# Kernel optimization log

Measured on AMD Instinct MI355X. Metric: run time of the kernel, lower is better.

The kernel has to match this reference:

```python
import jax, jax.numpy as jnp
import numpy as np

B, LQ, LK = 8, 1024, 1024
H, HD = 8, 128            # n_head, hidden_dim (per-head)
HEAD_DIM, CHILD_DIM = 512, 512
D_MODEL = HEAD_DIM + CHILD_DIM
TEMP = float(np.sqrt(HD))
NEG = 100000000.0
EPS = 1e-5


def setup_inputs() -> dict:
    key = jax.random.key(0)
    ks = jax.random.split(key, 12)
    q = jax.random.normal(ks[0], (B, LQ, HEAD_DIM), jnp.float32)
    k = jax.random.normal(ks[1], (B, LK, CHILD_DIM), jnp.float32)
    v = jax.random.normal(ks[2], (B, LK, D_MODEL), jnp.float32)
    old_score = 0.1 * jax.random.normal(ks[3], (H * B, LQ, LK), jnp.float32)
    float_mask = (jax.random.uniform(ks[4], (B, LQ, LK)) > 0.2).astype(jnp.float32)
    # torch nn.Linear weights are [out_features, in_features]
    wq = jax.random.normal(ks[5], (H * HD, HEAD_DIM), jnp.float32) * np.sqrt(2.0 / (HEAD_DIM + HD))
    wk = jax.random.normal(ks[6], (H * HD, CHILD_DIM), jnp.float32) * np.sqrt(2.0 / (CHILD_DIM + HD))
    wv = jax.random.normal(ks[7], (H * HD, D_MODEL), jnp.float32) * np.sqrt(2.0 / (D_MODEL + HD))
    wfc = jax.random.normal(ks[8], (D_MODEL, H * HD), jnp.float32) * np.sqrt(2.0 / (D_MODEL + H * HD))
    bq = jnp.zeros((H * HD,), jnp.float32)
    bk = jnp.zeros((H * HD,), jnp.float32)
    bv = jnp.zeros((H * HD,), jnp.float32)
    bfc = jnp.zeros((D_MODEL,), jnp.float32)
    ln_g = jnp.ones((D_MODEL,), jnp.float32)
    ln_b = jnp.zeros((D_MODEL,), jnp.float32)
    return dict(q=q, k=k, v=v, old_score=old_score, float_mask=float_mask,
                wq=wq, bq=bq, wk=wk, bk=bk, wv=wv, bv=bv,
                wfc=wfc, bfc=bfc, ln_g=ln_g, ln_b=ln_b)


def reference(q, k, v, old_score, float_mask, wq, bq, wk, bk, wv, bv, wfc, bfc, ln_g, ln_b):
    b, lq, _ = q.shape
    lk = k.shape[1]
    residual = v
    qh = (q @ wq.T + bq).reshape(b, lq, H, HD)   # [b,lq,h,d]
    kh = (k @ wk.T + bk).reshape(b, lk, H, HD)
    vh = (v @ wv.T + bv).reshape(b, lk, H, HD)
    # raw_score laid out head-major to match torch's (n_head*B, Lq, Lk)
    raw = jnp.einsum('bqhd,bkhd->hbqk', qh, kh) + old_score.reshape(H, b, lq, lk)
    score = raw - NEG * (1.0 - float_mask)[None]          # broadcast over heads
    attn = jax.nn.softmax(score / TEMP, axis=-1)          # eval path
    out = jnp.einsum('hbqk,bkhd->bqhd', attn, vh).reshape(b, lq, H * HD)
    out = out @ wfc.T + bfc + residual                    # dropout=identity (eval)
    mean = jnp.mean(out, axis=-1, keepdims=True)
    var = jnp.mean(jnp.square(out - mean), axis=-1, keepdims=True)
    out = (out - mean) / jnp.sqrt(var + EPS) * ln_g + ln_b
    return out, raw.reshape(H * b, lq, lk)
```

## Files before the change

### kernel.cpp

```cpp
#include <hip/hip_runtime.h>

typedef unsigned short u16;
typedef __bf16 bf16x8 __attribute__((ext_vector_type(8)));
typedef float f32x4 __attribute__((ext_vector_type(4)));

#define MFMA16(a,b,c) __builtin_amdgcn_mfma_f32_16x16x32_bf16(a,b,c,0,0,0)
#define WAITV(n) asm volatile("s_waitcnt vmcnt(" #n ")" ::: "memory")
#define SBAR()   __builtin_amdgcn_s_barrier()
#define SCHED0() __builtin_amdgcn_sched_barrier(0)

static __device__ __forceinline__ u16 f2bf(float f){
  unsigned u = __builtin_bit_cast(unsigned, f);
  u += 0x7fffu + ((u>>16)&1u);
  return (u16)(u>>16);
}
static __device__ __forceinline__ int swz256(int r,int c){ return r*256 + (c ^ ((r&7)<<4)); }
static __device__ __forceinline__ int swz128(int r,int c){ return r*128 + (c ^ ((r&7)<<4)); }

static __device__ __forceinline__ void gload16(const void* g, void* l){
  __builtin_amdgcn_global_load_lds(
      (const __attribute__((address_space(1))) unsigned int*)g,
      (__attribute__((address_space(3))) unsigned int*)l, 16, 0, 0);
}

__global__ void conv_f2b(const float* __restrict__ in, u16* __restrict__ out, int n4){
  int i = blockIdx.x*256 + threadIdx.x;
  if (i >= n4) return;
  float4 f = reinterpret_cast<const float4*>(in)[i];
  ushort4 o; o.x=f2bf(f.x); o.y=f2bf(f.y); o.z=f2bf(f.z); o.w=f2bf(f.w);
  reinterpret_cast<ushort4*>(out)[i] = o;
}

__global__ void mask2bits(const float* __restrict__ fm, unsigned char* __restrict__ bits){
  int i = blockIdx.x*256 + threadIdx.x;
  const float4* p = reinterpret_cast<const float4*>(fm + (size_t)i*8);
  float4 a = p[0], bq = p[1];
  unsigned v = 0;
  v |= (a.x  > 0.5f) ? 1u   : 0u;
  v |= (a.y  > 0.5f) ? 2u   : 0u;
  v |= (a.z  > 0.5f) ? 4u   : 0u;
  v |= (a.w  > 0.5f) ? 8u   : 0u;
  v |= (bq.x > 0.5f) ? 16u  : 0u;
  v |= (bq.y > 0.5f) ? 32u  : 0u;
  v |= (bq.z > 0.5f) ? 64u  : 0u;
  v |= (bq.w > 0.5f) ? 128u : 0u;
  bits[i] = (unsigned char)v;
}

template<int MODE>
__global__ __launch_bounds__(256) void gemm_nt(const u16* __restrict__ A, const u16* __restrict__ Bw,
    const float* __restrict__ bias, const float* __restrict__ resid,
    u16* __restrict__ Cb, float* __restrict__ Cf, int M, int N, int K)
{
  __shared__ uint4 ldsv[2048];
  char* la = (char*)ldsv;
  char* lb = la + 16384;
  const int tid = threadIdx.x, lane = tid&63, w = tid>>6;
  const int l15 = lane&15, l4 = lane>>4;
  const int wm = w&1, wn = w>>1;
  const int mb = blockIdx.x, nb = blockIdx.y;
  const f32x4 zero4 = {0.f,0.f,0.f,0.f};
  f32x4 acc[4][4];
  #pragma unroll
  for (int i=0;i<4;++i)
    #pragma unroll
    for (int j=0;j<4;++j) acc[i][j] = zero4;

  for (int k0=0;k0<K;k0+=64){
    __syncthreads();
    #pragma unroll
    for (int it=0; it<4; ++it){
      int slot = it*256 + tid;
      int r = slot>>3, cg = (slot&7) ^ (r&7);
      gload16(A + (size_t)(mb*128+r)*K + k0 + cg*8, la + (it*256 + w*64)*16);
      gload16(Bw + (size_t)(nb*128+r)*K + k0 + cg*8, lb + (it*256 + w*64)*16);
    }
    __syncthreads();
    #pragma unroll
    for (int kk=0;kk<2;++kk){
      bf16x8 af[4], bfr[4];
      #pragma unroll
      for (int i=0;i<4;++i){
        af[i]  = *reinterpret_cast<const bf16x8*>(la + swz128(wm*64+i*16+l15, (kk*32+l4*8)*2));
        bfr[i] = *reinterpret_cast<const bf16x8*>(lb + swz128(wn*64+i*16+l15, (kk*32+l4*8)*2));
      }
      #pragma unroll
      for (int i=0;i<4;++i)
        #pragma unroll
        for (int j=0;j<4;++j)
          acc[i][j] = MFMA16(af[i], bfr[j], acc[i][j]);
    }
  }
  #pragma unroll
  for (int j=0;j<4;++j){
    int col = nb*128 + wn*64 + j*16 + l15;
    float bv = bias[col];
    #pragma unroll
    for (int i=0;i<4;++i){
      int row0 = mb*128 + wm*64 + i*16 + l4*4;
      if (MODE == 0){
        #pragma unroll
        for (int r=0;r<4;++r)
          Cb[(size_t)(row0+r)*N + col] = f2bf(acc[i][j][r] + bv);
      } else if (MODE == 1){
        int bb = row0 >> 10, kp = row0 & 1023;
        ushort4 o;
        o.x = f2bf(acc[i][j][0]+bv); o.y = f2bf(acc[i][j][1]+bv);
        o.z = f2bf(acc[i][j][2]+bv); o.w = f2bf(acc[i][j][3]+bv);
        *reinterpret_cast<ushort4*>(Cb + (size_t)(bb*1024+col)*1024 + kp) = o;
      } else {
        #pragma unroll
        for (int r=0;r<4;++r){
          size_t off = (size_t)(row0+r)*N + col;
          Cf[off] = acc[i][j][r] + bv + resid[off];
        }
      }
    }
  }
}

__global__ __launch_bounds__(256) void attn_fused(const u16* __restrict__ qh,
    const u16* __restrict__ kh, const u16* __restrict__ vt,
    const float* __restrict__ oldsc, const unsigned char* __restrict__ bits,
    float* __restrict__ raw, u16* __restrict__ ao)
{
  __shared__ uint4 ldsv[4608];
  char* lk0 = (char*)ldsv;
  char* lv0 = lk0 + 16384;
  char* lk1 = lk0 + 32768;
  char* lv1 = lk0 + 49152;
  char* lp_ = lk0 + 65536;
  const int tid = threadIdx.x, lane = tid&63, w = tid>>6;
  const int l15 = lane&15, l4 = lane>>4;
  unsigned ublk = blockIdx.x;
  int slotid = (ublk & 7) * 128 + (ublk >> 3);
  const int qb = slotid & 15, bh = slotid >> 4;
  const int b = bh & 7, h = bh >> 3;
  const float invT = 0.088388347648318447f;
  const f32x4 zero4 = {0.f,0.f,0.f,0.f};

  const int qglob = qb*64 + w*16 + l4*4;
  const float* oldp = oldsc + ((size_t)(h*8+b)*1024 + qglob)*1024 + l15*4;
  float*       rawp = raw   + ((size_t)(h*8+b)*1024 + qglob)*1024 + l15*4;
  const unsigned char* bitp = bits + ((size_t)b*1024 + qglob)*128 + (l15>>1);
  const u16* khB = kh + (size_t)b*1024*1024 + h*128;
  const u16* vtB = vt + ((size_t)b*1024 + h*128)*1024;
  const int nsh = (l15&1)*4;

  bf16x8 qf[4];
  {
    const u16* qp = qh + (size_t)(b*1024 + qb*64 + w*16 + l15)*1024 + h*128 + l4*8;
    #pragma unroll
    for (int kk=0;kk<4;++kk)
      qf[kk] = __builtin_bit_cast(bf16x8, *reinterpret_cast<const uint4*>(qp + kk*32));
  }
  f32x4 oacc[8];
  #pragma unroll
  for (int i=0;i<8;++i) oacc[i] = zero4;
  float mr[4], lr[4];
  #pragma unroll
  for (int r=0;r<4;++r){ mr[r] = -3.0e38f; lr[r] = 0.f; }

  auto stage = [&](int kt, char* lkD, char* lvD){
    #pragma unroll
    for (int it=0; it<4; ++it){
      int slot = it*256 + tid;
      int rs = slot>>4, cs = slot&15;
      int ck = cs ^ (rs&7);
      int kv = (rs&15)*4 + (rs>>4);
      gload16(khB + (size_t)(kt*64 + kv)*1024 + ck*8, lkD + (it*256 + w*64)*16);
      int r8 = slot>>3, cgv = (slot&7) ^ (r8&7);
      gload16(vtB + (size_t)r8*1024 + kt*64 + cgv*8, lvD + (it*256 + w*64)*16);
    }
  };
  auto pref = [&](int kt, float4 (&o4)[4], unsigned char (&bb)[4]){
    #pragma unroll
    for (int r=0;r<4;++r){
      o4[r] = *reinterpret_cast<const float4*>(oldp + (size_t)r*1024 + kt*64);
      bb[r] = bitp[(size_t)r*128 + kt*8];
    }
  };
  auto body = [&](int kt, char* lkR, char* lvR, float4 (&o4)[4], unsigned char (&bb)[4]){
    f32x4 fs[4];
    #pragma unroll
    for (int fj=0;fj<4;++fj){
      f32x4 s = zero4;
      #pragma unroll
      for (int kk=0;kk<4;++kk){
        bf16x8 kf = *reinterpret_cast<const bf16x8*>(lkR + swz256(fj*16+l15, (kk*32+l4*8)*2));
        s = MFMA16(qf[kk], kf, s);
      }
      fs[fj] = s;
    }
    float tm[4];
    #pragma unroll
    for (int r=0;r<4;++r){
      float4 rv;
      rv.x = fs[0][r] + o4[r].x; rv.y = fs[1][r] + o4[r].y;
      rv.z = fs[2][r] + o4[r].z; rv.w = fs[3][r] + o4[r].w;
      *reinterpret_cast<float4*>(rawp + (size_t)r*1024 + kt*64) = rv;
      unsigned nib = ((unsigned)bb[r]) >> nsh;
      fs[0][r] = (rv.x - ((nib&1u) ? 0.f : 1.0e8f)) * invT;
      fs[1][r] = (rv.y - ((nib&2u) ? 0.f : 1.0e8f)) * invT;
      fs[2][r] = (rv.z - ((nib&4u) ? 0.f : 1.0e8f)) * invT;
      fs[3][r] = (rv.w - ((nib&8u) ? 0.f : 1.0e8f)) * invT;
      tm[r] = fmaxf(fmaxf(fs[0][r], fs[1][r]), fmaxf(fs[2][r], fs[3][r]));
    }
    #pragma unroll
    for (int o=1;o<16;o<<=1){
      #pragma unroll
      for (int r=0;r<4;++r) tm[r] = fmaxf(tm[r], __shfl_xor(tm[r], o));
    }
    #pragma unroll
    for (int r=0;r<4;++r){
      float mn  = fmaxf(mr[r], tm[r]);
      float esc = __expf(mr[r] - mn);
      mr[r] = mn;
      lr[r] *= esc;
      #pragma unroll
      for (int nf=0;nf<8;++nf) oacc[nf][r] *= esc;
      float px = __expf(fs[0][r] - mn), py = __expf(fs[1][r] - mn);
      float pz = __expf(fs[2][r] - mn), pw = __expf(fs[3][r] - mn);
      lr[r] += px + py + pz + pw;
      ushort4 o;
      o.x = f2bf(px); o.y = f2bf(py); o.z = f2bf(pz); o.w = f2bf(pw);
      int prow = w*16 + l4*4 + r;
      *reinterpret_cast<ushort4*>(lp_ + swz128(prow, l15*8)) = o;
    }
    #pragma unroll
    for (int kkv=0;kkv<2;++kkv){
      bf16x8 pf = *reinterpret_cast<const bf16x8*>(lp_ + swz128(w*16+l15, (kkv*32+l4*8)*2));
      #pragma unroll
      for (int nf=0;nf<8;++nf){
        bf16x8 vf = *reinterpret_cast<const bf16x8*>(lvR + swz128(nf*16+l15, (kkv*32+l4*8)*2));
        oacc[nf] = MFMA16(pf, vf, oacc[nf]);
      }
    }
  };

  float4 oA[4], oB[4];
  unsigned char bA[4], bB[4];
  stage(0, lk0, lv0);
  stage(1, lk1, lv1);
  pref(0, oA, bA);
  pref(1, oB, bB);
  WAITV(8);
  SBAR(); SCHED0();
  body(0, lk0, lv0, oA, bA);
  pref(2, oA, bA);

  #pragma unroll 1
  for (int t = 1; t <= 13; t += 2){
    SBAR();
    stage(t+1, lk0, lv0);
    WAITV(16);
    SBAR(); SCHED0();
    body(t, lk1, lv1, oB, bB);
    if (t+2 <= 15) pref(t+2, oB, bB);
    SBAR();
    stage(t+2, lk1, lv1);
    WAITV(16);
    SBAR(); SCHED0();
    body(t+1, lk0, lv0, oA, bA);
    if (t+3 <= 15) pref(t+3, oA, bA);
  }
  SBAR();
  WAITV(0);
  SBAR(); SCHED0();
  body(15, lk1, lv1, oB, bB);

  #pragma unroll
  for (int o=1;o<16;o<<=1){
    #pragma unroll
    for (int r=0;r<4;++r) lr[r] += __shfl_xor(lr[r], o);
  }
  #pragma unroll
  for (int nf=0;nf<8;++nf){
    int col = h*128 + nf*16 + l15;
    #pragma unroll
    for (int r=0;r<4;++r){
      size_t orow = (size_t)(b*1024 + qb*64 + w*16 + l4*4 + r);
      ao[orow*1024 + col] = f2bf(oacc[nf][r] * (1.0f/lr[r]));
    }
  }
}

__global__ __launch_bounds__(256) void ln_k(float* __restrict__ io,
    const float* __restrict__ g, const float* __restrict__ bb)
{
  const int lane = threadIdx.x & 63, w = threadIdx.x >> 6;
  size_t row = (size_t)blockIdx.x*4 + w;
  float4* p = reinterpret_cast<float4*>(io + row*1024);
  float4 x[4];
  float s = 0.f, s2 = 0.f;
  #pragma unroll
  for (int i=0;i<4;++i){
    x[i] = p[lane + i*64];
    s  += x[i].x + x[i].y + x[i].z + x[i].w;
    s2 += x[i].x*x[i].x + x[i].y*x[i].y + x[i].z*x[i].z + x[i].w*x[i].w;
  }
  #pragma unroll
  for (int o=1;o<64;o<<=1){ s += __shfl_xor(s,o); s2 += __shfl_xor(s2,o); }
  float mean = s * 0.0009765625f;
  float var  = s2 * 0.0009765625f - mean*mean;
  float rstd = rsqrtf(var + 1e-5f);
  const float4* gp = reinterpret_cast<const float4*>(g);
  const float4* bp = reinterpret_cast<const float4*>(bb);
  #pragma unroll
  for (int i=0;i<4;++i){
    float4 gg = gp[lane+i*64], bv = bp[lane+i*64], y;
    y.x = (x[i].x-mean)*rstd*gg.x + bv.x;
    y.y = (x[i].y-mean)*rstd*gg.y + bv.y;
    y.z = (x[i].z-mean)*rstd*gg.z + bv.z;
    y.w = (x[i].w-mean)*rstd*gg.w + bv.w;
    p[lane+i*64] = y;
  }
}

extern "C" void kernel_launch(void* const* d_in, const int* in_sizes, int n_in,
                              void* d_out, int out_size, void* d_ws, size_t ws_size,
                              hipStream_t stream)
{
  const float* q    = (const float*)d_in[0];
  const float* k    = (const float*)d_in[1];
  const float* v    = (const float*)d_in[2];
  const float* olds = (const float*)d_in[3];
  const float* fm   = (const float*)d_in[4];
  const float* wq   = (const float*)d_in[5];
  const float* bq   = (const float*)d_in[6];
  const float* wk   = (const float*)d_in[7];
  const float* bk   = (const float*)d_in[8];
  const float* wv   = (const float*)d_in[9];
  const float* bv   = (const float*)d_in[10];
  const float* wfc  = (const float*)d_in[11];
  const float* bfc  = (const float*)d_in[12];
  const float* lng  = (const float*)d_in[13];
  const float* lnb  = (const float*)d_in[14];
  float* out = (float*)d_out;
  float* raw = out + 8388608;

  u16* ws  = (u16*)d_ws;
  u16* qbf = ws;
  u16* kbf = qbf + 4194304;
  u16* vbf = kbf + 4194304;
  u16* wqb = vbf + 8388608;
  u16* wkb = wqb + 524288;
  u16* wvb = wkb + 524288;
  u16* wfb = wvb + 1048576;
  u16* qhb = wfb + 1048576;
  u16* khb = qhb + 8388608;
  u16* vtb = khb + 8388608;
  u16* aob = vtb + 8388608;
  unsigned char* bits = (unsigned char*)(aob + 8388608);

  conv_f2b<<<4096,256,0,stream>>>(q,   qbf, 1048576);
  conv_f2b<<<4096,256,0,stream>>>(k,   kbf, 1048576);
  conv_f2b<<<8192,256,0,stream>>>(v,   vbf, 2097152);
  conv_f2b<<<512, 256,0,stream>>>(wq,  wqb, 131072);
  conv_f2b<<<512, 256,0,stream>>>(wk,  wkb, 131072);
  conv_f2b<<<1024,256,0,stream>>>(wv,  wvb, 262144);
  conv_f2b<<<1024,256,0,stream>>>(wfc, wfb, 262144);
  mask2bits<<<4096,256,0,stream>>>(fm, bits);

  gemm_nt<0><<<dim3(64,8),256,0,stream>>>(qbf, wqb, bq, nullptr, qhb, nullptr, 8192,1024,512);
  gemm_nt<0><<<dim3(64,8),256,0,stream>>>(kbf, wkb, bk, nullptr, khb, nullptr, 8192,1024,512);
  gemm_nt<1><<<dim3(64,8),256,0,stream>>>(vbf, wvb, bv, nullptr, vtb, nullptr, 8192,1024,1024);

  attn_fused<<<1024,256,0,stream>>>(qhb, khb, vtb, olds, bits, raw, aob);

  gemm_nt<2><<<dim3(64,8),256,0,stream>>>(aob, wfb, bfc, v, nullptr, out, 8192,1024,1024);
  ln_k<<<2048,256,0,stream>>>(out, lng, lnb);
}
```

Baseline: 303.4 us.

## Repack mask bits per column group, deepen prefetch, skip uneeded softmax rescales

The mask bit layout changes so each lane fetches one 32-bit word holding four rows' bits instead of four separate byte loads. The fused attention loop now prefetches old_score and mask three tiles ahead with a third register set, unrolled by six, to hide global load latency. The online softmax skips the running-max update and accumulator rescale when no row's new max exceeds the old by more than 8, which trades a small exponent headroom for fewer multiplies. The changes add register pressure and more intricate vmcnt wait counts that must match the number of loads in flight.

Measured after the change: 331.2 us. 1.09x slower.

```diff
diff --git a/kernel.cpp b/kernel.cpp
--- a/kernel.cpp
+++ b/kernel.cpp
@@ -31,20 +31,30 @@
   reinterpret_cast<ushort4*>(out)[i] = o;
 }
 
-__global__ void mask2bits(const float* __restrict__ fm, unsigned char* __restrict__ bits){
-  int i = blockIdx.x*256 + threadIdx.x;
-  const float4* p = reinterpret_cast<const float4*>(fm + (size_t)i*8);
-  float4 a = p[0], bq = p[1];
-  unsigned v = 0;
-  v |= (a.x  > 0.5f) ? 1u   : 0u;
-  v |= (a.y  > 0.5f) ? 2u   : 0u;
-  v |= (a.z  > 0.5f) ? 4u   : 0u;
-  v |= (a.w  > 0.5f) ? 8u   : 0u;
-  v |= (bq.x > 0.5f) ? 16u  : 0u;
-  v |= (bq.y > 0.5f) ? 32u  : 0u;
-  v |= (bq.z > 0.5f) ? 64u  : 0u;
-  v |= (bq.w > 0.5f) ? 128u : 0u;
-  bits[i] = (unsigned char)v;
+__global__ void mask2bits(const float* __restrict__ fm, unsigned* __restrict__ bitsW){
+  int T = blockIdx.x*256 + threadIdx.x;
+  int c = T & 127;
+  int q4g = (T >> 7) & 255;
+  int b = T >> 15;
+  int q0 = q4g*4;
+  const float* src = fm + ((size_t)(b*1024 + q0))*1024 + c*8;
+  unsigned out = 0;
+  #pragma unroll
+  for (int r=0;r<4;++r){
+    const float4* p = reinterpret_cast<const float4*>(src + (size_t)r*1024);
+    float4 a = p[0], bq = p[1];
+    unsigned v = 0;
+    v |= (a.x  > 0.5f) ? 1u   : 0u;
+    v |= (a.y  > 0.5f) ? 2u   : 0u;
+    v |= (a.z  > 0.5f) ? 4u   : 0u;
+    v |= (a.w  > 0.5f) ? 8u   : 0u;
+    v |= (bq.x > 0.5f) ? 16u  : 0u;
+    v |= (bq.y > 0.5f) ? 32u  : 0u;
+    v |= (bq.z > 0.5f) ? 64u  : 0u;
+    v |= (bq.w > 0.5f) ? 128u : 0u;
+    out |= v << (r*8);
+  }
+  bitsW[(size_t)(b*128 + c)*256 + q4g] = out;
 }
 
 template<int MODE>
@@ -142,7 +152,7 @@
   const int qglob = qb*64 + w*16 + l4*4;
   const float* oldp = oldsc + ((size_t)(h*8+b)*1024 + qglob)*1024 + l15*4;
   float*       rawp = raw   + ((size_t)(h*8+b)*1024 + qglob)*1024 + l15*4;
-  const unsigned char* bitp = bits + ((size_t)b*1024 + qglob)*128 + (l15>>1);
+  const unsigned char* bitbase = bits + (size_t)b*131072 + (l15>>1)*1024 + qglob;
   const u16* khB = kh + (size_t)b*1024*1024 + h*128;
   const u16* vtB = vt + ((size_t)b*1024 + h*128)*1024;
   const int nsh = (l15&1)*4;
@@ -159,7 +169,7 @@
   for (int i=0;i<8;++i) oacc[i] = zero4;
   float mr[4], lr[4];
   #pragma unroll
-  for (int r=0;r<4;++r){ mr[r] = -3.0e38f; lr[r] = 0.f; }
+  for (int r=0;r<4;++r){ mr[r] = -1.0e30f; lr[r] = 0.f; }
 
   auto stage = [&](int kt, char* lkD, char* lvD){
     #pragma unroll
@@ -173,14 +183,13 @@
       gload16(vtB + (size_t)r8*1024 + kt*64 + cgv*8, lvD + (it*256 + w*64)*16);
     }
   };
-  auto pref = [&](int kt, float4 (&o4)[4], unsigned char (&bb)[4]){
-    #pragma unroll
-    for (int r=0;r<4;++r){
+  auto pref = [&](int kt, float4 (&o4)[4], unsigned &bw){
+    #pragma unroll
+    for (int r=0;r<4;++r)
       o4[r] = *reinterpret_cast<const float4*>(oldp + (size_t)r*1024 + kt*64);
-      bb[r] = bitp[(size_t)r*128 + kt*8];
-    }
+    bw = *reinterpret_cast<const unsigned*>(bitbase + (size_t)kt*8192);
   };
-  auto body = [&](int kt, char* lkR, char* lvR, float4 (&o4)[4], unsigned char (&bb)[4]){
+  auto body = [&](int kt, char* lkR, char* lvR, float4 (&o4)[4], unsigned bw){
     f32x4 fs[4];
     #pragma unroll
     for (int fj=0;fj<4;++fj){
@@ -199,7 +208,7 @@
       rv.x = fs[0][r] + o4[r].x; rv.y = fs[1][r] + o4[r].y;
       rv.z = fs[2][r] + o4[r].z; rv.w = fs[3][r] + o4[r].w;
       *reinterpret_cast<float4*>(rawp + (size_t)r*1024 + kt*64) = rv;
-      unsigned nib = ((unsigned)bb[r]) >> nsh;
+      unsigned nib = bw >> (r*8 + nsh);
       fs[0][r] = (rv.x - ((nib&1u) ? 0.f : 1.0e8f)) * invT;
       fs[1][r] = (rv.y - ((nib&2u) ? 0.f : 1.0e8f)) * invT;
       fs[2][r] = (rv.z - ((nib&4u) ? 0.f : 1.0e8f)) * invT;
@@ -211,16 +220,22 @@
       #pragma unroll
       for (int r=0;r<4;++r) tm[r] = fmaxf(tm[r], __shfl_xor(tm[r], o));
     }
+    float dmax = fmaxf(fmaxf(tm[0]-mr[0], tm[1]-mr[1]), fmaxf(tm[2]-mr[2], tm[3]-mr[3]));
+    if (!__all((int)(dmax <= 8.0f))){
+      #pragma unroll
+      for (int r=0;r<4;++r){
+        float mn  = fmaxf(mr[r], tm[r]);
+        float esc = __expf(mr[r] - mn);
+        lr[r] *= esc;
+        #pragma unroll
+        for (int nf=0;nf<8;++nf) oacc[nf][r] *= esc;
+        mr[r] = mn;
+      }
+    }
     #pragma unroll
     for (int r=0;r<4;++r){
-      float mn  = fmaxf(mr[r], tm[r]);
-      float esc = __expf(mr[r] - mn);
-      mr[r] = mn;
-      lr[r] *= esc;
-      #pragma unroll
-      for (int nf=0;nf<8;++nf) oacc[nf][r] *= esc;
-      float px = __expf(fs[0][r] - mn), py = __expf(fs[1][r] - mn);
-      float pz = __expf(fs[2][r] - mn), pw = __expf(fs[3][r] - mn);
+      float px = __expf(fs[0][r] - mr[r]), py = __expf(fs[1][r] - mr[r]);
+      float pz = __expf(fs[2][r] - mr[r]), pw = __expf(fs[3][r] - mr[r]);
       lr[r] += px + py + pz + pw;
       ushort4 o;
       o.x = f2bf(px); o.y = f2bf(py); o.z = f2bf(pz); o.w = f2bf(pw);
@@ -238,36 +253,47 @@
     }
   };
 
-  float4 oA[4], oB[4];
-  unsigned char bA[4], bB[4];
+  float4 oA[4], oB[4], oC[4];
+  unsigned bwA, bwB, bwC;
+
   stage(0, lk0, lv0);
   stage(1, lk1, lv1);
-  pref(0, oA, bA);
-  pref(1, oB, bB);
-  WAITV(8);
+  pref(0, oA, bwA);
+  pref(1, oB, bwB);
+  pref(2, oC, bwC);
+  WAITV(10);
   SBAR(); SCHED0();
-  body(0, lk0, lv0, oA, bA);
-  pref(2, oA, bA);
+  body(0, lk0, lv0, oA, bwA);
+  pref(3, oA, bwA);
+
+  SBAR();
+  stage(2, lk0, lv0);
+  WAITV(17); SBAR(); SCHED0();
+  body(1, lk1, lv1, oB, bwB);
+  pref(4, oB, bwB);
+
+#define ATT_STEP(T, LKr, LVr, LKs, LVs, OS, BWS, DOPREF) \
+  SBAR(); stage((T)+1, LKs, LVs); WAITV(17); SBAR(); SCHED0(); \
+  body((T), LKr, LVr, OS, BWS); if (DOPREF) pref((T)+3, OS, BWS);
 
   #pragma unroll 1
-  for (int t = 1; t <= 13; t += 2){
-    SBAR();
-    stage(t+1, lk0, lv0);
-    WAITV(16);
-    SBAR(); SCHED0();
-    body(t, lk1, lv1, oB, bB);
-    if (t+2 <= 15) pref(t+2, oB, bB);
-    SBAR();
-    stage(t+2, lk1, lv1);
-    WAITV(16);
-    SBAR(); SCHED0();
-    body(t+1, lk0, lv0, oA, bA);
-    if (t+3 <= 15) pref(t+3, oA, bA);
-  }
+  for (int tb = 2; tb <= 8; tb += 6){
+    ATT_STEP(tb+0, lk0,lv0, lk1,lv1, oC,bwC, true)
+    ATT_STEP(tb+1, lk1,lv1, lk0,lv0, oA,bwA, true)
+    ATT_STEP(tb+2, lk0,lv0, lk1,lv1, oB,bwB, true)
+    ATT_STEP(tb+3, lk1,lv1, lk0,lv0, oC,bwC, true)
+    ATT_STEP(tb+4, lk0,lv0, lk1,lv1, oA,bwA, true)
+    ATT_STEP(tb+5, lk1,lv1, lk0,lv0, oB,bwB, (tb+8 <= 15))
+  }
+#undef ATT_STEP
+
   SBAR();
-  WAITV(0);
-  SBAR(); SCHED0();
-  body(15, lk1, lv1, oB, bB);
+  stage(15, lk1, lv1);
+  WAITV(12); SBAR(); SCHED0();
+  body(14, lk0, lv0, oC, bwC);
+  SBAR();
+  WAITV(4); SBAR(); SCHED0();
+  body(15, lk1, lv1, oA, bwA);
 
   #pragma unroll
   for (int o=1;o<16;o<<=1){
@@ -360,7 +386,7 @@
   conv_f2b<<<512, 256,0,stream>>>(wk,  wkb, 131072);
   conv_f2b<<<1024,256,0,stream>>>(wv,  wvb, 262144);
   conv_f2b<<<1024,256,0,stream>>>(wfc, wfb, 262144);
-  mask2bits<<<4096,256,0,stream>>>(fm, bits);
+  mask2bits<<<1024,256,0,stream>>>(fm, (unsigned*)bits);
 
   gemm_nt<0><<<dim3(64,8),256,0,stream>>>(qbf, wqb, bq, nullptr, qhb, nullptr, 8192,1024,512);
   gemm_nt<0><<<dim3(64,8),256,0,stream>>>(kbf, wkb, bk, nullptr, khb, nullptr, 8192,1024,512);
```

## Software-pipeline attention: overlap QK of next tile with PV of previous

Applied to the files above, without the earlier changes.

Restructures the attention loop so the K and V tiles are staged separately and the P·V product of tile t-1 runs alongside the QK product of tile t, with double-buffered P in LDS. It also adds a lazy-rescale rule that skips the online-softmax rescale of the accumulators when the wavefront's max grows by at most 8, and merges four weight-conversion launches into a single kernel. The aim is to hide the softmax and barrier latency behind matrix-core work and to cut launch overhead. The cost is more LDS per block, which can lower occupancy, and more complex wait-count bookkeeping.

New measurement: 329.3 us. 8.5% more time.

```diff
diff --git a/kernel.cpp b/kernel.cpp
--- a/kernel.cpp
+++ b/kernel.cpp
@@ -29,6 +29,21 @@
   float4 f = reinterpret_cast<const float4*>(in)[i];
   ushort4 o; o.x=f2bf(f.x); o.y=f2bf(f.y); o.z=f2bf(f.z); o.w=f2bf(f.w);
   reinterpret_cast<ushort4*>(out)[i] = o;
+}
+
+__global__ void conv_w(const float* __restrict__ wq, const float* __restrict__ wk,
+                       const float* __restrict__ wv, const float* __restrict__ wfc,
+                       u16* __restrict__ wqb, u16* __restrict__ wkb,
+                       u16* __restrict__ wvb, u16* __restrict__ wfb){
+  int i = blockIdx.x*256 + threadIdx.x;
+  const float* s; u16* d; int off;
+  if (i < 131072)      { s=wq;  d=wqb; off=i; }
+  else if (i < 262144) { s=wk;  d=wkb; off=i-131072; }
+  else if (i < 524288) { s=wv;  d=wvb; off=i-262144; }
+  else                 { s=wfc; d=wfb; off=i-524288; }
+  float4 f = reinterpret_cast<const float4*>(s)[off];
+  ushort4 o; o.x=f2bf(f.x); o.y=f2bf(f.y); o.z=f2bf(f.z); o.w=f2bf(f.w);
+  reinterpret_cast<ushort4*>(d)[off] = o;
 }
 
 __global__ void mask2bits(const float* __restrict__ fm, unsigned char* __restrict__ bits){
@@ -124,12 +139,13 @@
     const float* __restrict__ oldsc, const unsigned char* __restrict__ bits,
     float* __restrict__ raw, u16* __restrict__ ao)
 {
-  __shared__ uint4 ldsv[4608];
+  __shared__ uint4 ldsv[5120];
   char* lk0 = (char*)ldsv;
-  char* lv0 = lk0 + 16384;
-  char* lk1 = lk0 + 32768;
+  char* lk1 = lk0 + 16384;
+  char* lv0 = lk0 + 32768;
   char* lv1 = lk0 + 49152;
-  char* lp_ = lk0 + 65536;
+  char* lp0 = lk0 + 65536;
+  char* lp1 = lk0 + 73728;
   const int tid = threadIdx.x, lane = tid&63, w = tid>>6;
   const int l15 = lane&15, l4 = lane>>4;
   unsigned ublk = blockIdx.x;
@@ -161,7 +177,7 @@
   #pragma unroll
   for (int r=0;r<4;++r){ mr[r] = -3.0e38f; lr[r] = 0.f; }
 
-  auto stage = [&](int kt, char* lkD, char* lvD){
+  auto stageK = [&](int kt, char* lkD){
     #pragma unroll
     for (int it=0; it<4; ++it){
       int slot = it*256 + tid;
@@ -169,6 +185,12 @@
       int ck = cs ^ (rs&7);
       int kv = (rs&15)*4 + (rs>>4);
       gload16(khB + (size_t)(kt*64 + kv)*1024 + ck*8, lkD + (it*256 + w*64)*16);
+    }
+  };
+  auto stageV = [&](int kt, char* lvD){
+    #pragma unroll
+    for (int it=0; it<4; ++it){
+      int slot = it*256 + tid;
       int r8 = slot>>3, cgv = (slot&7) ^ (r8&7);
       gload16(vtB + (size_t)r8*1024 + kt*64 + cgv*8, lvD + (it*256 + w*64)*16);
     }
@@ -180,8 +202,7 @@
       bb[r] = bitp[(size_t)r*128 + kt*8];
     }
   };
-  auto body = [&](int kt, char* lkR, char* lvR, float4 (&o4)[4], unsigned char (&bb)[4]){
-    f32x4 fs[4];
+  auto qk = [&](char* lkR, f32x4 (&fs)[4]){
     #pragma unroll
     for (int fj=0;fj<4;++fj){
       f32x4 s = zero4;
@@ -192,6 +213,19 @@
       }
       fs[fj] = s;
     }
+  };
+  auto pv = [&](char* lvR, char* lpR){
+    #pragma unroll
+    for (int kkv=0;kkv<2;++kkv){
+      bf16x8 pf = *reinterpret_cast<const bf16x8*>(lpR + swz128(w*16+l15, (kkv*32+l4*8)*2));
+      #pragma unroll
+      for (int nf=0;nf<8;++nf){
+        bf16x8 vf = *reinterpret_cast<const bf16x8*>(lvR + swz128(nf*16+l15, (kkv*32+l4*8)*2));
+        oacc[nf] = MFMA16(pf, vf, oacc[nf]);
+      }
+    }
+  };
+  auto sm = [&](int kt, f32x4 (&fs)[4], float4 (&o4)[4], unsigned char (&bb)[4], char* lpW){
     float tm[4];
     #pragma unroll
     for (int r=0;r<4;++r){
@@ -211,63 +245,79 @@
       #pragma unroll
       for (int r=0;r<4;++r) tm[r] = fmaxf(tm[r], __shfl_xor(tm[r], o));
     }
+    float dmax = fmaxf(fmaxf(tm[0]-mr[0], tm[1]-mr[1]), fmaxf(tm[2]-mr[2], tm[3]-mr[3]));
+    if (!__all((int)(dmax <= 8.0f))){
+      #pragma unroll
+      for (int r=0;r<4;++r){
+        float mn  = fmaxf(mr[r], tm[r]);
+        float esc = __expf(mr[r] - mn);
+        lr[r] *= esc;
+        #pragma unroll
+        for (int nf=0;nf<8;++nf) oacc[nf][r] *= esc;
+        mr[r] = mn;
+      }
+    }
     #pragma unroll
     for (int r=0;r<4;++r){
-      float mn  = fmaxf(mr[r], tm[r]);
-      float esc = __expf(mr[r] - mn);
-      mr[r] = mn;
-      lr[r] *= esc;
-      #pragma unroll
-      for (int nf=0;nf<8;++nf) oacc[nf][r] *= esc;
-      float px = __expf(fs[0][r] - mn), py = __expf(fs[1][r] - mn);
-      float pz = __expf(fs[2][r] - mn), pw = __expf(fs[3][r] - mn);
+      float px = __expf(fs[0][r] - mr[r]), py = __expf(fs[1][r] - mr[r]);
+      float pz = __expf(fs[2][r] - mr[r]), pw = __expf(fs[3][r] - mr[r]);
       lr[r] += px + py + pz + pw;
       ushort4 o;
       o.x = f2bf(px); o.y = f2bf(py); o.z = f2bf(pz); o.w = f2bf(pw);
       int prow = w*16 + l4*4 + r;
-      *reinterpret_cast<ushort4*>(lp_ + swz128(prow, l15*8)) = o;
-    }
-    #pragma unroll
-    for (int kkv=0;kkv<2;++kkv){
-      bf16x8 pf = *reinterpret_cast<const bf16x8*>(lp_ + swz128(w*16+l15, (kkv*32+l4*8)*2));
-      #pragma unroll
-      for (int nf=0;nf<8;++nf){
-        bf16x8 vf = *reinterpret_cast<const bf16x8*>(lvR + swz128(nf*16+l15, (kkv*32+l4*8)*2));
-        oacc[nf] = MFMA16(pf, vf, oacc[nf]);
-      }
+      *reinterpret_cast<ushort4*>(lpW + swz128(prow, l15*8)) = o;
     }
   };
 
   float4 oA[4], oB[4];
   unsigned char bA[4], bB[4];
-  stage(0, lk0, lv0);
-  stage(1, lk1, lv1);
+
+  stageK(0, lk0);
   pref(0, oA, bA);
   pref(1, oB, bB);
-  WAITV(8);
+  WAITV(10);
   SBAR(); SCHED0();
-  body(0, lk0, lv0, oA, bA);
-  pref(2, oA, bA);
+
+  {
+    stageK(1, lk1); stageV(0, lv0); SCHED0();
+    f32x4 fs[4];
+    qk(lk0, fs);
+    sm(0, fs, oA, bA, lp0);
+    pref(2, oA, bA);
+    WAITV(9); SBAR(); SCHED0();
+  }
 
   #pragma unroll 1
   for (int t = 1; t <= 13; t += 2){
-    SBAR();
-    stage(t+1, lk0, lv0);
-    WAITV(16);
-    SBAR(); SCHED0();
-    body(t, lk1, lv1, oB, bB);
-    if (t+2 <= 15) pref(t+2, oB, bB);
-    SBAR();
-    stage(t+2, lk1, lv1);
-    WAITV(16);
-    SBAR(); SCHED0();
-    body(t+1, lk0, lv0, oA, bA);
-    if (t+3 <= 15) pref(t+3, oA, bA);
-  }
-  SBAR();
-  WAITV(0);
-  SBAR(); SCHED0();
-  body(15, lk1, lv1, oB, bB);
+    {
+      stageK(t+1, lk0); stageV(t, lv1); SCHED0();
+      f32x4 fs[4];
+      qk(lk1, fs);
+      pv(lv0, lp0);
+      sm(t, fs, oB, bB, lp1);
+      pref(t+2, oB, bB);
+      WAITV(9); SBAR(); SCHED0();
+    }
+    {
+      stageK(t+2, lk1); stageV(t+1, lv0); SCHED0();
+      f32x4 fs[4];
+      qk(lk0, fs);
+      pv(lv1, lp1);
+      sm(t+1, fs, oA, bA, lp0);
+      pref(t+3 <= 15 ? t+3 : 15, oA, bA);
+      WAITV(9); SBAR(); SCHED0();
+    }
+  }
+
+  {
+    stageV(15, lv1); SCHED0();
+    f32x4 fs[4];
+    qk(lk1, fs);
+    pv(lv0, lp0);
+    sm(15, fs, oB, bB, lp1);
+    WAITV(4); SBAR(); SCHED0();
+    pv(lv1, lp1);
+  }
 
   #pragma unroll
   for (int o=1;o<16;o<<=1){
@@ -356,10 +406,7 @@
   conv_f2b<<<4096,256,0,stream>>>(q,   qbf, 1048576);
   conv_f2b<<<4096,256,0,stream>>>(k,   kbf, 1048576);
   conv_f2b<<<8192,256,0,stream>>>(v,   vbf, 2097152);
-  conv_f2b<<<512, 256,0,stream>>>(wq,  wqb, 131072);
-  conv_f2b<<<512, 256,0,stream>>>(wk,  wkb, 131072);
-  conv_f2b<<<1024,256,0,stream>>>(wv,  wvb, 262144);
-  conv_f2b<<<1024,256,0,stream>>>(wfc, wfb, 262144);
+  conv_w<<<3072,256,0,stream>>>(wq, wk, wv, wfc, wqb, wkb, wvb, wfb);
   mask2bits<<<4096,256,0,stream>>>(fm, bits);
 
   gemm_nt<0><<<dim3(64,8),256,0,stream>>>(qbf, wqb, bq, nullptr, qhb, nullptr, 8192,1024,512);
```

## Process two 64-row query tiles per attention block and merge weight conversions

Applied to the files above, without the earlier changes.

Each attention workgroup now handles 128 query rows as two independent 64-row halves that share every staged K/V tile in LDS. This halves the number of blocks and halves K/V global traffic per query row. The cost is doubled accumulator and softmax-state registers, with launch bounds raised to request two blocks per CU. Separately, the four weight fp32-to-bf16 conversion launches are folded into one kernel to cut launch overhead.

New measurement: 516.7 us. 70.3% more time.

```diff
diff --git a/kernel.cpp b/kernel.cpp
--- a/kernel.cpp
+++ b/kernel.cpp
@@ -29,6 +29,21 @@
   float4 f = reinterpret_cast<const float4*>(in)[i];
   ushort4 o; o.x=f2bf(f.x); o.y=f2bf(f.y); o.z=f2bf(f.z); o.w=f2bf(f.w);
   reinterpret_cast<ushort4*>(out)[i] = o;
+}
+
+__global__ void conv_w(const float* __restrict__ wq, const float* __restrict__ wk,
+                       const float* __restrict__ wv, const float* __restrict__ wfc,
+                       u16* __restrict__ wqb, u16* __restrict__ wkb,
+                       u16* __restrict__ wvb, u16* __restrict__ wfb){
+  int i = blockIdx.x*256 + threadIdx.x;
+  const float* s; u16* d; int off;
+  if (i < 131072)      { s=wq;  d=wqb; off=i; }
+  else if (i < 262144) { s=wk;  d=wkb; off=i-131072; }
+  else if (i < 524288) { s=wv;  d=wvb; off=i-262144; }
+  else                 { s=wfc; d=wfb; off=i-524288; }
+  float4 f = reinterpret_cast<const float4*>(s)[off];
+  ushort4 o; o.x=f2bf(f.x); o.y=f2bf(f.y); o.z=f2bf(f.z); o.w=f2bf(f.w);
+  reinterpret_cast<ushort4*>(d)[off] = o;
 }
 
 __global__ void mask2bits(const float* __restrict__ fm, unsigned char* __restrict__ bits){
@@ -119,7 +134,7 @@
   }
 }
 
-__global__ __launch_bounds__(256) void attn_fused(const u16* __restrict__ qh,
+__global__ __launch_bounds__(256, 2) void attn_fused(const u16* __restrict__ qh,
     const u16* __restrict__ kh, const u16* __restrict__ vt,
     const float* __restrict__ oldsc, const unsigned char* __restrict__ bits,
     float* __restrict__ raw, u16* __restrict__ ao)
@@ -133,33 +148,36 @@
   const int tid = threadIdx.x, lane = tid&63, w = tid>>6;
   const int l15 = lane&15, l4 = lane>>4;
   unsigned ublk = blockIdx.x;
-  int slotid = (ublk & 7) * 128 + (ublk >> 3);
-  const int qb = slotid & 15, bh = slotid >> 4;
+  int slotid = (ublk & 7) * 64 + (ublk >> 3);
+  const int qb = slotid & 7, bh = slotid >> 3;
   const int b = bh & 7, h = bh >> 3;
   const float invT = 0.088388347648318447f;
   const f32x4 zero4 = {0.f,0.f,0.f,0.f};
 
-  const int qglob = qb*64 + w*16 + l4*4;
-  const float* oldp = oldsc + ((size_t)(h*8+b)*1024 + qglob)*1024 + l15*4;
-  float*       rawp = raw   + ((size_t)(h*8+b)*1024 + qglob)*1024 + l15*4;
-  const unsigned char* bitp = bits + ((size_t)b*1024 + qglob)*128 + (l15>>1);
+  const int qgA = qb*128 + w*16 + l4*4;
+  const size_t rbaseA = ((size_t)(h*8+b)*1024 + qgA)*1024 + l15*4;
+  const float* oldp = oldsc + rbaseA;
+  float*       rawp = raw   + rbaseA;
+  const unsigned char* bitp = bits + ((size_t)b*1024 + qgA)*128 + (l15>>1);
   const u16* khB = kh + (size_t)b*1024*1024 + h*128;
   const u16* vtB = vt + ((size_t)b*1024 + h*128)*1024;
   const int nsh = (l15&1)*4;
 
-  bf16x8 qf[4];
+  bf16x8 qfA[4], qfB[4];
   {
-    const u16* qp = qh + (size_t)(b*1024 + qb*64 + w*16 + l15)*1024 + h*128 + l4*8;
-    #pragma unroll
-    for (int kk=0;kk<4;++kk)
-      qf[kk] = __builtin_bit_cast(bf16x8, *reinterpret_cast<const uint4*>(qp + kk*32));
-  }
-  f32x4 oacc[8];
-  #pragma unroll
-  for (int i=0;i<8;++i) oacc[i] = zero4;
-  float mr[4], lr[4];
-  #pragma unroll
-  for (int r=0;r<4;++r){ mr[r] = -3.0e38f; lr[r] = 0.f; }
+    const u16* qpA = qh + (size_t)(b*1024 + qb*128 + w*16 + l15)*1024 + h*128 + l4*8;
+    #pragma unroll
+    for (int kk=0;kk<4;++kk){
+      qfA[kk] = __builtin_bit_cast(bf16x8, *reinterpret_cast<const uint4*>(qpA + kk*32));
+      qfB[kk] = __builtin_bit_cast(bf16x8, *reinterpret_cast<const uint4*>(qpA + (size_t)64*1024 + kk*32));
+    }
+  }
+  f32x4 oaccA[8], oaccB[8];
+  #pragma unroll
+  for (int i=0;i<8;++i){ oaccA[i] = zero4; oaccB[i] = zero4; }
+  float mrA[4], lrA[4], mrB[4], lrB[4];
+  #pragma unroll
+  for (int r=0;r<4;++r){ mrA[r] = -3.0e38f; lrA[r] = 0.f; mrB[r] = -3.0e38f; lrB[r] = 0.f; }
 
   auto stage = [&](int kt, char* lkD, char* lvD){
     #pragma unroll
@@ -173,14 +191,20 @@
       gload16(vtB + (size_t)r8*1024 + kt*64 + cgv*8, lvD + (it*256 + w*64)*16);
     }
   };
-  auto pref = [&](int kt, float4 (&o4)[4], unsigned char (&bb)[4]){
+  auto prefAB = [&](int kt, float4 (&oa)[4], unsigned char (&ba)[4],
+                            float4 (&ob)[4], unsigned char (&bb)[4]){
     #pragma unroll
     for (int r=0;r<4;++r){
-      o4[r] = *reinterpret_cast<const float4*>(oldp + (size_t)r*1024 + kt*64);
-      bb[r] = bitp[(size_t)r*128 + kt*8];
+      oa[r] = *reinterpret_cast<const float4*>(oldp + (size_t)r*1024 + kt*64);
+      ob[r] = *reinterpret_cast<const float4*>(oldp + (size_t)(r+64)*1024 + kt*64);
+      ba[r] = bitp[(size_t)r*128 + kt*8];
+      bb[r] = bitp[(size_t)(r+64)*128 + kt*8];
     }
   };
-  auto body = [&](int kt, char* lkR, char* lvR, float4 (&o4)[4], unsigned char (&bb)[4]){
+
+  auto half = [&](int kt, char* lkR, char* lvR, const bf16x8 (&qf)[4],
+                  f32x4 (&oacc)[8], float (&mr)[4], float (&lr)[4],
+                  float4 (&o4)[4], unsigned char (&bb)[4], int roff){
     f32x4 fs[4];
     #pragma unroll
     for (int fj=0;fj<4;++fj){
@@ -198,7 +222,7 @@
       float4 rv;
       rv.x = fs[0][r] + o4[r].x; rv.y = fs[1][r] + o4[r].y;
       rv.z = fs[2][r] + o4[r].z; rv.w = fs[3][r] + o4[r].w;
-      *reinterpret_cast<float4*>(rawp + (size_t)r*1024 + kt*64) = rv;
+      *reinterpret_cast<float4*>(rawp + (size_t)(r+roff)*1024 + kt*64) = rv;
       unsigned nib = ((unsigned)bb[r]) >> nsh;
       fs[0][r] = (rv.x - ((nib&1u) ? 0.f : 1.0e8f)) * invT;
       fs[1][r] = (rv.y - ((nib&2u) ? 0.f : 1.0e8f)) * invT;
@@ -237,50 +261,58 @@
       }
     }
   };
-
-  float4 oA[4], oB[4];
-  unsigned char bA[4], bB[4];
+  auto body = [&](int kt, char* lkR, char* lvR,
+                  float4 (&oa)[4], unsigned char (&ba)[4],
+                  float4 (&ob)[4], unsigned char (&bb)[4]){
+    half(kt, lkR, lvR, qfA, oaccA, mrA, lrA, oa, ba, 0);
+    half(kt, lkR, lvR, qfB, oaccB, mrB, lrB, ob, bb, 64);
+  };
+
+  float4 oXa[4], oXb[4], oYa[4], oYb[4];
+  unsigned char bXa[4], bXb[4], bYa[4], bYb[4];
+
   stage(0, lk0, lv0);
   stage(1, lk1, lv1);
-  pref(0, oA, bA);
-  pref(1, oB, bB);
-  WAITV(8);
+  prefAB(0, oXa, bXa, oXb, bXb);
+  prefAB(1, oYa, bYa, oYb, bYb);
+  WAITV(10);
   SBAR(); SCHED0();
-  body(0, lk0, lv0, oA, bA);
-  pref(2, oA, bA);
+  body(0, lk0, lv0, oXa, bXa, oXb, bXb);
+  prefAB(2, oXa, bXa, oXb, bXb);
 
   #pragma unroll 1
   for (int t = 1; t <= 13; t += 2){
     SBAR();
     stage(t+1, lk0, lv0);
-    WAITV(16);
+    WAITV(18);
     SBAR(); SCHED0();
-    body(t, lk1, lv1, oB, bB);
-    if (t+2 <= 15) pref(t+2, oB, bB);
+    body(t, lk1, lv1, oYa, bYa, oYb, bYb);
+    if (t+2 <= 15) prefAB(t+2, oYa, bYa, oYb, bYb);
     SBAR();
     stage(t+2, lk1, lv1);
-    WAITV(16);
+    WAITV(18);
     SBAR(); SCHED0();
-    body(t+1, lk0, lv0, oA, bA);
-    if (t+3 <= 15) pref(t+3, oA, bA);
+    body(t+1, lk0, lv0, oXa, bXa, oXb, bXb);
+    if (t+3 <= 15) prefAB(t+3, oXa, bXa, oXb, bXb);
   }
   SBAR();
   WAITV(0);
   SBAR(); SCHED0();
-  body(15, lk1, lv1, oB, bB);
+  body(15, lk1, lv1, oYa, bYa, oYb, bYb);
 
   #pragma unroll
   for (int o=1;o<16;o<<=1){
     #pragma unroll
-    for (int r=0;r<4;++r) lr[r] += __shfl_xor(lr[r], o);
+    for (int r=0;r<4;++r){ lrA[r] += __shfl_xor(lrA[r], o); lrB[r] += __shfl_xor(lrB[r], o); }
   }
   #pragma unroll
   for (int nf=0;nf<8;++nf){
     int col = h*128 + nf*16 + l15;
     #pragma unroll
     for (int r=0;r<4;++r){
-      size_t orow = (size_t)(b*1024 + qb*64 + w*16 + l4*4 + r);
-      ao[orow*1024 + col] = f2bf(oacc[nf][r] * (1.0f/lr[r]));
+      size_t orowA = (size_t)(b*1024 + qb*128 + w*16 + l4*4 + r);
+      ao[orowA*1024 + col]            = f2bf(oaccA[nf][r] * (1.0f/lrA[r]));
+      ao[(orowA+64)*1024 + col]       = f2bf(oaccB[nf][r] * (1.0f/lrB[r]));
     }
   }
 }
@@ -356,17 +388,14 @@
   conv_f2b<<<4096,256,0,stream>>>(q,   qbf, 1048576);
   conv_f2b<<<4096,256,0,stream>>>(k,   kbf, 1048576);
   conv_f2b<<<8192,256,0,stream>>>(v,   vbf, 2097152);
-  conv_f2b<<<512, 256,0,stream>>>(wq,  wqb, 131072);
-  conv_f2b<<<512, 256,0,stream>>>(wk,  wkb, 131072);
-  conv_f2b<<<1024,256,0,stream>>>(wv,  wvb, 262144);
-  conv_f2b<<<1024,256,0,stream>>>(wfc, wfb, 262144);
+  conv_w<<<3072,256,0,stream>>>(wq, wk, wv, wfc, wqb, wkb, wvb, wfb);
   mask2bits<<<4096,256,0,stream>>>(fm, bits);
 
   gemm_nt<0><<<dim3(64,8),256,0,stream>>>(qbf, wqb, bq, nullptr, qhb, nullptr, 8192,1024,512);
   gemm_nt<0><<<dim3(64,8),256,0,stream>>>(kbf, wkb, bk, nullptr, khb, nullptr, 8192,1024,512);
   gemm_nt<1><<<dim3(64,8),256,0,stream>>>(vbf, wvb, bv, nullptr, vtb, nullptr, 8192,1024,1024);
 
-  attn_fused<<<1024,256,0,stream>>>(qhb, khb, vtb, olds, bits, raw, aob);
+  attn_fused<<<512,256,0,stream>>>(qhb, khb, vtb, olds, bits, raw, aob);
 
   gemm_nt<2><<<dim3(64,8),256,0,stream>>>(aob, wfb, bfc, v, nullptr, out, 8192,1024,1024);
   ln_k<<<2048,256,0,stream>>>(out, lng, lnb);
```
